# Optimization experiments

Measured on AMD Instinct MI355X. Metric: run time of the kernel, lower is better.

## Reference

```python
import jax, jax.numpy as jnp
import numpy as np

N_VARS = 32
D_MODEL = 256
D_MECH = 128
D_NOISE = D_MODEL // 4
N_LAYERS = 3
TEMP = 0.5
BATCH = 512


def gelu(x):
    return jax.nn.gelu(x, approximate=False)  # torch nn.GELU default is exact erf


def setup_inputs() -> dict:
    key = jax.random.key(0)
    ks = jax.random.split(key, 12)
    n, d, m, dn = N_VARS, D_MODEL, D_MECH, D_NOISE
    return {
        "exogenous_noise": jax.random.normal(ks[0], (BATCH, n, dn), dtype=jnp.float32),
        # learned params (edge_logits init randn*0.5 for a nontrivial adjacency)
        "edge_logits": jax.random.normal(ks[1], (n, n), dtype=jnp.float32) * 0.5,
        "var_emb": jax.random.normal(ks[2], (n, d), dtype=jnp.float32) * 0.02,
        # shared parent_aggregate Linear(d, d); weights stored [in, out]
        "pa_W": jax.random.normal(ks[3], (d, d), dtype=jnp.float32) / np.sqrt(d).astype(np.float32),
        "pa_b": jnp.zeros((d,), dtype=jnp.float32),
        # per-variable mechanism MLP weights, stacked on variable axis
        "m_W1": jax.random.normal(ks[4], (n, d, m), dtype=jnp.float32) / np.sqrt(d).astype(np.float32),
        "m_b1": jnp.zeros((n, m), dtype=jnp.float32),
        "m_W2": jax.random.normal(ks[5], (n, m, m), dtype=jnp.float32) / np.sqrt(m).astype(np.float32),
        "m_b2": jnp.zeros((n, m), dtype=jnp.float32),
        "m_W3": jax.random.normal(ks[6], (n, m, d), dtype=jnp.float32) / np.sqrt(m).astype(np.float32),
        "m_b3": jnp.zeros((n, d), dtype=jnp.float32),
        # per-variable noise encoder Linear(dn, d)
        "ne_W": jax.random.normal(ks[7], (n, dn, d), dtype=jnp.float32) / np.sqrt(dn).astype(np.float32),
        "ne_b": jnp.zeros((n, d), dtype=jnp.float32),
    }


def _forward(exogenous_noise, edge_logits, var_emb, pa_W, pa_b,
             m_W1, m_b1, m_W2, m_b2, m_W3, m_b3, ne_W, ne_b):
    n, d = N_VARS, D_MODEL
    batch = exogenous_noise.shape[0]
    # eval-mode adjacency: sigmoid(masked_logits / temp); diagonal masked out
    diag_mask = 1.0 - jnp.eye(n, dtype=edge_logits.dtype)
    adj = jax.nn.sigmoid((edge_logits * diag_mask) / jnp.asarray(TEMP, edge_logits.dtype))
    adj_cols = adj.T                                  # row i = adj[:, i], parents of var i
    noise_t = jnp.transpose(exogenous_noise, (1, 0, 2))  # (n, batch, dn)

    values0 = jnp.zeros((batch, n, d), dtype=exogenous_noise.dtype)
    idx = jnp.arange(n)
    xs = (idx, adj_cols, var_emb, noise_t, m_W1, m_b1, m_W2, m_b2, m_W3, m_b3, ne_W, ne_b)

    def var_step(values, x):
        i, a_col, emb_i, nz, w1, b1, w2, b2, w3, b3, nw, nb = x
        # adjacency-weighted aggregation over ALL current values (sequentially updated)
        pc = jnp.einsum('v,bvd->bd', a_col, values)
        parent_input = gelu((pc + emb_i) @ pa_W + pa_b)
        h = gelu(parent_input @ w1 + b1)
        h = gelu(h @ w2 + b2)
        out = h @ w3 + b3
        out = out + gelu(nz @ nw + nb)               # noise encoder contribution
        values = values.at[:, i].set(out)
        return values, None

    values = values0
    for _ in range(N_LAYERS):
        values, _ = jax.lax.scan(var_step, values, xs)
    return values


def reference(exogenous_noise, edge_logits, var_emb, pa_W, pa_b,
              m_W1, m_b1, m_W2, m_b2, m_W3, m_b3, ne_W, ne_b):
    return _forward(exogenous_noise, edge_logits, var_emb, pa_W, pa_b,
                    m_W1, m_b1, m_W2, m_b2, m_W3, m_b3, ne_W, ne_b)
```

## Files before the change

kernel.cpp:

```cpp
#include <hip/hip_runtime.h>


typedef __bf16 bf16x8 __attribute__((ext_vector_type(8)));
typedef float  f32x4  __attribute__((ext_vector_type(4)));

#define N_VARS 32
#define BTILE 4
#define NBLK 128

#define WS_ADJB   0
#define WS_B3P    4096
#define WS_EMBP   36864
#define WS_WSB    69632
#define ELOFF_PA  0
#define ELOFF_W1  65536
#define ELOFF_W2  1114112
#define ELOFF_W3  1638400
#define ELOFF_W3P 2686976
#define WS_NE2    7540736

#define XSTR 272
#define HSTR 144
#define VSTR 40

__device__ __forceinline__ unsigned short f2b(float f) {
    unsigned u = __float_as_uint(f);
    u += 0x7FFFu + ((u >> 16) & 1u);
    return (unsigned short)(u >> 16);
}

__device__ __forceinline__ float b2f(unsigned short u) {
    return __uint_as_float(((unsigned)u) << 16);
}

__device__ __forceinline__ void bar_lds() {
    asm volatile("s_waitcnt lgkmcnt(0)\n\ts_barrier" ::: "memory");
}

__device__ __forceinline__ float gelu_e(float x) {
    float z  = x * 0.7071067811865476f;
    float az = fabsf(z);
    float t  = __builtin_amdgcn_rcpf(1.0f + 0.47047f * az);
    float p  = t * (0.3480242f + t * (-0.0958798f + t * 0.7478556f));
    float e  = 1.0f - p * __expf(-z * z);
    float er = (z < 0.0f) ? -e : e;
    return 0.5f * x * (1.0f + er);
}

__device__ __forceinline__ float pickq(f32x4 v, int q) {
    float lo = (q & 1) ? v[1] : v[0];
    float hi = (q & 1) ? v[3] : v[2];
    return (q & 2) ? hi : lo;
}
__device__ __forceinline__ float pick4(float x0, float x1, float x2, float x3, int q) {
    float lo = (q & 1) ? x1 : x0;
    float hi = (q & 1) ? x3 : x2;
    return (q & 2) ? hi : lo;
}

#define MFMA16(a, b, c) __builtin_amdgcn_mfma_f32_16x16x32_bf16(a, b, c, 0, 0, 0)

__global__ void prep_lin(const float* __restrict__ paW, const float* __restrict__ mW3,
                         const float* __restrict__ mb3, const float* __restrict__ emb,
                         const float* __restrict__ pab,
                         float* __restrict__ tmpf, float* __restrict__ b3P,
                         float* __restrict__ embP) {
    const int b = blockIdx.x, d = threadIdx.x;
    if (b < 512) {
        const int v = b >> 4, mg = (b & 15) * 8;
        const float* w3r = mW3 + (size_t)(v * 128 + mg) * 256;
        float acc[8];
        #pragma unroll
        for (int r = 0; r < 8; r++) acc[r] = 0.f;
        for (int n = 0; n < 256; n++) {
            float pa = paW[n * 256 + d];
            #pragma unroll
            for (int r = 0; r < 8; r++) acc[r] += w3r[r * 256 + n] * pa;
        }
        #pragma unroll
        for (int r = 0; r < 8; r++)
            tmpf[(size_t)(v * 128 + mg + r) * 256 + d] = acc[r];
    } else if (b < 544) {
        const int v = b - 512;
        float a = 0.f;
        for (int n = 0; n < 256; n++) a += mb3[v * 256 + n] * paW[n * 256 + d];
        b3P[v * 256 + d] = a;
    } else {
        const int v = b - 544;
        float a = pab[d];
        for (int n = 0; n < 256; n++) a += emb[v * 256 + n] * paW[n * 256 + d];
        embP[v * 256 + d] = a;
    }
}

__global__ void prep_all(const float* __restrict__ paW, const float* __restrict__ mW1,
                         const float* __restrict__ mW2, const float* __restrict__ mW3,
                         const float* __restrict__ edge, unsigned short* __restrict__ wsb,
                         unsigned short* __restrict__ adjb,
                         const float* __restrict__ noise, const float* __restrict__ neW,
                         const float* __restrict__ neb, float* __restrict__ outp,
                         const float* __restrict__ tmpf) {
    __shared__ unsigned short tile[32 * 256];
    const int c = blockIdx.x, tid = threadIdx.x;
    if (c < 648) {
        const float* src; unsigned short* dst; int N, KS, ks;
        if (c < 8)        { src = paW;                     dst = wsb + ELOFF_PA;              N = 256; KS = 8; ks = c; }
        else if (c < 264) { int v = (c - 8) >> 3;   ks = (c - 8) & 7;
                            src = mW1 + v * 32768;         dst = wsb + ELOFF_W1 + v * 32768;  N = 128; KS = 8; }
        else if (c < 392) { int v = (c - 264) >> 2; ks = (c - 264) & 3;
                            src = mW2 + v * 16384;         dst = wsb + ELOFF_W2 + v * 16384;  N = 128; KS = 4; }
        else if (c < 520) { int v = (c - 392) >> 2; ks = (c - 392) & 3;
                            src = mW3 + v * 32768;         dst = wsb + ELOFF_W3 + v * 32768;  N = 256; KS = 4; }
        else              { int v = (c - 520) >> 2; ks = (c - 520) & 3;
                            src = tmpf + v * 32768;        dst = wsb + ELOFF_W3P + v * 32768; N = 256; KS = 4; }
        const int kb = ks * 32, nsh = (N == 256) ? 8 : 7;
        for (int t = tid; t < 32 * N; t += 256) {
            int r = t >> nsh, col = t & (N - 1);
            tile[r * N + col] = f2b(src[(kb + r) * N + col]);
        }
        __syncthreads();
        const int nout = (N >> 4) * 64;
        for (int o = tid; o < nout; o += 256) {
            int nt = o >> 6, lane = o & 63;
            int n = nt * 16 + (lane & 15), k0 = (lane >> 4) << 3;
            unsigned e[8];
            #pragma unroll
            for (int j = 0; j < 8; j++) e[j] = tile[(k0 + j) * N + n];
            uint4 pk;
            pk.x = e[0] | (e[1] << 16); pk.y = e[2] | (e[3] << 16);
            pk.z = e[4] | (e[5] << 16); pk.w = e[6] | (e[7] << 16);
            *(uint4*)(dst + ((nt * KS + ks) * 64 + lane) * 8) = pk;
        }
    } else if (c == 648) {
        for (int t = tid; t < 1024; t += 256) {
            int v = t >> 5, ci = t & 31;
            float x = edge[t];
            float m = (v == ci) ? 0.0f : x;
            float a = __builtin_amdgcn_rcpf(1.0f + __expf(-2.0f * m));
            unsigned short hi = f2b(a);
            float rem = a - b2f(hi);
            adjb[ci * 64 + v]      = hi;
            adjb[ci * 64 + 32 + v] = f2b(rem);
        }
    } else {
        int sb = c - 649;
        int i = sb >> 5, g = sb & 31, d = tid;
        float w[64];
        #pragma unroll
        for (int k = 0; k < 64; k++) w[k] = neW[(i * 64 + k) * 256 + d];
        float bias = neb[i * 256 + d];
        for (int bb = 0; bb < 16; bb++) {
            int b = g * 16 + bb;
            const float* nr = noise + (b * 32 + i) * 64;
            float a0 = bias, a1 = 0.f, a2 = 0.f, a3 = 0.f;
            #pragma unroll
            for (int k = 0; k < 16; k++) {
                a0 += nr[4 * k + 0] * w[4 * k + 0];
                a1 += nr[4 * k + 1] * w[4 * k + 1];
                a2 += nr[4 * k + 2] * w[4 * k + 2];
                a3 += nr[4 * k + 3] * w[4 * k + 3];
            }
            outp[(b * 32 + i) * 256 + d] = gelu_e((a0 + a1) + (a2 + a3));
        }
    }
}

__global__ void prep_ne2(const float* __restrict__ nep, const __bf16* __restrict__ wsbf,
                         unsigned short* __restrict__ ne2) {
    const int tid = threadIdx.x;
    const int wid = tid >> 6, lane = tid & 63, l15 = lane & 15, q = lane >> 4;
    const int gt = blockIdx.x * 4 + wid;
    const int rowbase = gt * 16;
    bf16x8 afr[8];
    #pragma unroll
    for (int ks = 0; ks < 8; ks++) {
        const float* s = nep + (size_t)(rowbase + l15) * 256 + ks * 32 + q * 8;
        float4 x0 = *(const float4*)s;
        float4 x1 = *(const float4*)(s + 4);
        uint4 pk;
        pk.x = (unsigned)f2b(x0.x) | ((unsigned)f2b(x0.y) << 16);
        pk.y = (unsigned)f2b(x0.z) | ((unsigned)f2b(x0.w) << 16);
        pk.z = (unsigned)f2b(x1.x) | ((unsigned)f2b(x1.y) << 16);
        pk.w = (unsigned)f2b(x1.z) | ((unsigned)f2b(x1.w) << 16);
        afr[ks] = __builtin_bit_cast(bf16x8, pk);
    }
    #pragma unroll 4
    for (int nt = 0; nt < 16; nt++) {
        f32x4 e4 = {0, 0, 0, 0}, o4 = {0, 0, 0, 0};
        #pragma unroll
        for (int ks = 0; ks < 8; ks += 2) {
            bf16x8 b0 = *(const bf16x8*)(wsbf + ELOFF_PA + ((nt * 8 + ks) * 64 + lane) * 8);
            bf16x8 b1 = *(const bf16x8*)(wsbf + ELOFF_PA + ((nt * 8 + ks + 1) * 64 + lane) * 8);
            e4 = MFMA16(afr[ks], b0, e4);
            o4 = MFMA16(afr[ks + 1], b1, o4);
        }
        f32x4 a = e4 + o4;
        #pragma unroll
        for (int r = 0; r < 4; r++)
            ne2[(size_t)(rowbase + 4 * q + r) * 256 + nt * 16 + l15] = f2b(a[r]);
    }
}

__global__ __launch_bounds__(512) void
scm_main(const float* __restrict__ embP, const float* __restrict__ b3Pp,
         const float* __restrict__ mb1, const float* __restrict__ mb2,
         const float* __restrict__ mb3, const unsigned short* __restrict__ adjb,
         const __bf16* __restrict__ wsbf, const unsigned short* __restrict__ ne2,
         float* __restrict__ outp) {
    __shared__ unsigned short valsP[1024 * VSTR];
    __shared__ unsigned short X2[4 * XSTR];
    __shared__ unsigned short Hs1[4 * HSTR];
    __shared__ unsigned short Hs2[4 * HSTR];

    const int tid = threadIdx.x, blk = blockIdx.x;

    {
        uint4 z; z.x = z.y = z.z = z.w = 0;
        for (int k = tid; k < 5120; k += 512) ((uint4*)valsP)[k] = z;
    }

    const int wid = tid >> 6, lane = tid & 63, l15 = lane & 15, q = lane >> 4;
    const int l3 = l15 & 3;
    const int nW = wid * 16 + l15;
    const int n0 = nW, n1 = nW + 128;

    X2[q * XSTR + n0] = f2b(gelu_e(embP[n0]));
    X2[q * XSTR + n1] = f2b(gelu_e(embP[n1]));
    bar_lds();

    for (int s = 0; s < 3 * N_VARS; s++) {
        const int i = s & 31, ni = (s + 1) & 31;
        const bool last = s >= 64;

        float bi1 = mb1[i * 128 + nW];
        float bi2 = mb2[i * 128 + nW];
        bf16x8 w1f[8];
        #pragma unroll
        for (int ks = 0; ks < 8; ks++)
            w1f[ks] = *(const bf16x8*)(wsbf + ELOFF_W1 + (size_t)i * 32768 +
                                       ((wid * 8 + ks) * 64 + lane) * 8);
        bf16x8 w2f[4], wPf0[4], wPf1[4];
        #pragma unroll
        for (int ks = 0; ks < 4; ks++) {
            w2f[ks]  = *(const bf16x8*)(wsbf + ELOFF_W2 + (size_t)i * 16384 +
                                        ((wid * 4 + ks) * 64 + lane) * 8);
            wPf0[ks] = *(const bf16x8*)(wsbf + ELOFF_W3P + (size_t)i * 32768 +
                                        ((wid * 4 + ks) * 64 + lane) * 8);
            wPf1[ks] = *(const bf16x8*)(wsbf + ELOFF_W3P + (size_t)i * 32768 +
                                        (((wid + 8) * 4 + ks) * 64 + lane) * 8);
        }
        const size_t nrow = ((size_t)(blk * BTILE + q) * 32 + i) * 256;
        const float ne2_0 = b2f(ne2[nrow + n0]);
        const float ne2_1 = b2f(ne2[nrow + n1]);
        const float b3P0 = b3Pp[i * 256 + n0];
        const float b3P1 = b3Pp[i * 256 + n1];
        const float eP0 = embP[ni * 256 + n0];
        const float eP1 = embP[ni * 256 + n1];
        bf16x8 anh = *(const bf16x8*)(adjb + ni * 64 + q * 8);
        bf16x8 anl = *(const bf16x8*)(adjb + ni * 64 + 32 + q * 8);
        const float ani = b2f(adjb[ni * 64 + i]) + b2f(adjb[ni * 64 + 32 + i]);
        bf16x8 w3f0[4], w3f1[4];
        float b3a = 0.f, b3b = 0.f, neq0 = 0.f, neq1 = 0.f;
        if (last) {
            #pragma unroll
            for (int ks = 0; ks < 4; ks++) {
                w3f0[ks] = *(const bf16x8*)(wsbf + ELOFF_W3 + (size_t)i * 32768 +
                                            ((wid * 4 + ks) * 64 + lane) * 8);
                w3f1[ks] = *(const bf16x8*)(wsbf + ELOFF_W3 + (size_t)i * 32768 +
                                            (((wid + 8) * 4 + ks) * 64 + lane) * 8);
            }
            b3a = mb3[i * 256 + n0];
            b3b = mb3[i * 256 + n1];
            neq0 = outp[nrow + n0];
            neq1 = outp[nrow + n1];
        }

        {
            f32x4 aa = {0, 0, 0, 0}, ab = {0, 0, 0, 0};
            f32x4 ac = {0, 0, 0, 0}, ad = {0, 0, 0, 0};
            #pragma unroll
            for (int ks = 0; ks < 8; ks += 4) {
                bf16x8 af0 = *(const bf16x8*)(X2 + l3 * XSTR + ks * 32 + q * 8);
                bf16x8 af1 = *(const bf16x8*)(X2 + l3 * XSTR + (ks + 1) * 32 + q * 8);
                bf16x8 af2 = *(const bf16x8*)(X2 + l3 * XSTR + (ks + 2) * 32 + q * 8);
                bf16x8 af3 = *(const bf16x8*)(X2 + l3 * XSTR + (ks + 3) * 32 + q * 8);
                aa = MFMA16(af0, w1f[ks], aa);
                ab = MFMA16(af1, w1f[ks + 1], ab);
                ac = MFMA16(af2, w1f[ks + 2], ac);
                ad = MFMA16(af3, w1f[ks + 3], ad);
            }
            float sb = (pickq(aa, q) + pickq(ab, q)) +
                       (pickq(ac, q) + pickq(ad, q)) + bi1;
            Hs1[q * HSTR + nW] = f2b(gelu_e(sb));
        }
        bar_lds();

        f32x4 P0[4], P1[4];
        float oP0, oP1;
        {
            f32x4 ca = {0, 0, 0, 0}, cb = {0, 0, 0, 0};
            #pragma unroll
            for (int ks = 0; ks < 4; ks += 2) {
                bf16x8 af0 = *(const bf16x8*)(Hs1 + l3 * HSTR + ks * 32 + q * 8);
                bf16x8 af1 = *(const bf16x8*)(Hs1 + l3 * HSTR + (ks + 1) * 32 + q * 8);
                ca = MFMA16(af0, w2f[ks], ca);
                cb = MFMA16(af1, w2f[ks + 1], cb);
            }
            #pragma unroll
            for (int t = 0; t < 4; t++) {
                bf16x8 vf0 = *(const bf16x8*)(valsP + (t * 256 + n0) * VSTR + q * 8);
                bf16x8 vf1 = *(const bf16x8*)(valsP + (t * 256 + n1) * VSTR + q * 8);
                f32x4 z = {0, 0, 0, 0};
                P0[t] = MFMA16(anl, vf0, MFMA16(anh, vf0, z));
                P1[t] = MFMA16(anl, vf1, MFMA16(anh, vf1, z));
            }
            oP0 = b2f(valsP[(q * 256 + n0) * VSTR + i]);
            oP1 = b2f(valsP[(q * 256 + n1) * VSTR + i]);
            float scv = pickq(ca, q) + pickq(cb, q) + bi2;
            Hs2[q * HSTR + nW] = f2b(gelu_e(scv));
        }
        bar_lds();

        {
            f32x4 c0a = {0, 0, 0, 0}, c0b = {0, 0, 0, 0};
            f32x4 c1a = {0, 0, 0, 0}, c1b = {0, 0, 0, 0};
            #pragma unroll
            for (int ks = 0; ks < 4; ks += 2) {
                bf16x8 af0 = *(const bf16x8*)(Hs2 + l3 * HSTR + ks * 32 + q * 8);
                bf16x8 af1 = *(const bf16x8*)(Hs2 + l3 * HSTR + (ks + 1) * 32 + q * 8);
                c0a = MFMA16(af0, wPf0[ks], c0a);
                c1a = MFMA16(af0, wPf1[ks], c1a);
                c0b = MFMA16(af1, wPf0[ks + 1], c0b);
                c1b = MFMA16(af1, wPf1[ks + 1], c1b);
            }
            float nP0 = pickq(c0a, q) + pickq(c0b, q) + b3P0 + ne2_0;
            float nP1 = pickq(c1a, q) + pickq(c1b, q) + b3P1 + ne2_1;
            unsigned short ur0 = f2b(nP0), ur1 = f2b(nP1);
            valsP[(q * 256 + n0) * VSTR + i] = ur0;
            valsP[(q * 256 + n1) * VSTR + i] = ur1;
            float pc0 = pick4(P0[0][0], P0[1][0], P0[2][0], P0[3][0], q);
            float pc1 = pick4(P1[0][0], P1[1][0], P1[2][0], P1[3][0], q);
            float x0 = pc0 + ani * (b2f(ur0) - oP0) + eP0;
            float x1 = pc1 + ani * (b2f(ur1) - oP1) + eP1;
            X2[q * XSTR + n0] = f2b(gelu_e(x0));
            X2[q * XSTR + n1] = f2b(gelu_e(x1));
            if (last) {
                f32x4 d0a = {0, 0, 0, 0}, d0b = {0, 0, 0, 0};
                f32x4 d1a = {0, 0, 0, 0}, d1b = {0, 0, 0, 0};
                #pragma unroll
                for (int ks = 0; ks < 4; ks += 2) {
                    bf16x8 af0 = *(const bf16x8*)(Hs2 + l3 * HSTR + ks * 32 + q * 8);
                    bf16x8 af1 = *(const bf16x8*)(Hs2 + l3 * HSTR + (ks + 1) * 32 + q * 8);
                    d0a = MFMA16(af0, w3f0[ks], d0a);
                    d1a = MFMA16(af0, w3f1[ks], d1a);
                    d0b = MFMA16(af1, w3f0[ks + 1], d0b);
                    d1b = MFMA16(af1, w3f1[ks + 1], d1b);
                }
                outp[nrow + n0] = pickq(d0a, q) + pickq(d0b, q) + b3a + neq0;
                outp[nrow + n1] = pickq(d1a, q) + pickq(d1b, q) + b3b + neq1;
            }
        }
        bar_lds();
    }
}

extern "C" void kernel_launch(void* const* d_in, const int* in_sizes, int n_in,
                              void* d_out, int out_size, void* d_ws, size_t ws_size,
                              hipStream_t stream) {
    (void)in_sizes; (void)n_in; (void)out_size; (void)ws_size;
    const float* noise = (const float*)d_in[0];
    const float* edge  = (const float*)d_in[1];
    const float* emb   = (const float*)d_in[2];
    const float* paW   = (const float*)d_in[3];
    const float* pab   = (const float*)d_in[4];
    const float* mW1   = (const float*)d_in[5];
    const float* mb1   = (const float*)d_in[6];
    const float* mW2   = (const float*)d_in[7];
    const float* mb2   = (const float*)d_in[8];
    const float* mW3   = (const float*)d_in[9];
    const float* mb3   = (const float*)d_in[10];
    const float* neW   = (const float*)d_in[11];
    const float* neb   = (const float*)d_in[12];
    float* outp = (float*)d_out;

    unsigned short* adjb = (unsigned short*)((char*)d_ws + WS_ADJB);
    float* b3P  = (float*)((char*)d_ws + WS_B3P);
    float* embP = (float*)((char*)d_ws + WS_EMBP);
    unsigned short* wsb  = (unsigned short*)((char*)d_ws + WS_WSB);
    float* tmpf = (float*)((char*)d_ws + WS_NE2);
    unsigned short* ne2u = (unsigned short*)((char*)d_ws + WS_NE2);

    prep_lin<<<576, 256, 0, stream>>>(paW, mW3, mb3, emb, pab, tmpf, b3P, embP);
    prep_all<<<1673, 256, 0, stream>>>(paW, mW1, mW2, mW3, edge, wsb, adjb,
                                       noise, neW, neb, outp, tmpf);
    prep_ne2<<<256, 256, 0, stream>>>(outp, (const __bf16*)wsb, ne2u);
    scm_main<<<NBLK, 512, 0, stream>>>(embP, b3P, mb1, mb2, mb3, adjb,
                                       (const __bf16*)wsb, ne2u, outp);
}
```

Measured before the change: 424.1 us.

## Merge prep_lin into prep_all and double-buffer per-variable weights in main loop

Folds the W3·paW product, the b3 and embedding projections into the single prep_all launch, writing the W3P product straight into the MFMA fragment layout in bf16 and dropping the fp32 tmp buffer and one kernel launch. In the sequential 96-step main loop, the next variable's W1/W2/W3P fragments are prefetched into a second register set while the current step runs, so global weight-load latency is hidden behind compute. This doubles weight register usage, which may raise register pressure or cause spills.

```diff
diff --git a/kernel.cpp b/kernel.cpp
--- a/kernel.cpp
+++ b/kernel.cpp
@@ -60,59 +60,26 @@
 
 #define MFMA16(a, b, c) __builtin_amdgcn_mfma_f32_16x16x32_bf16(a, b, c, 0, 0, 0)
 
-__global__ void prep_lin(const float* __restrict__ paW, const float* __restrict__ mW3,
-                         const float* __restrict__ mb3, const float* __restrict__ emb,
-                         const float* __restrict__ pab,
-                         float* __restrict__ tmpf, float* __restrict__ b3P,
-                         float* __restrict__ embP) {
-    const int b = blockIdx.x, d = threadIdx.x;
-    if (b < 512) {
-        const int v = b >> 4, mg = (b & 15) * 8;
-        const float* w3r = mW3 + (size_t)(v * 128 + mg) * 256;
-        float acc[8];
-        #pragma unroll
-        for (int r = 0; r < 8; r++) acc[r] = 0.f;
-        for (int n = 0; n < 256; n++) {
-            float pa = paW[n * 256 + d];
-            #pragma unroll
-            for (int r = 0; r < 8; r++) acc[r] += w3r[r * 256 + n] * pa;
-        }
-        #pragma unroll
-        for (int r = 0; r < 8; r++)
-            tmpf[(size_t)(v * 128 + mg + r) * 256 + d] = acc[r];
-    } else if (b < 544) {
-        const int v = b - 512;
-        float a = 0.f;
-        for (int n = 0; n < 256; n++) a += mb3[v * 256 + n] * paW[n * 256 + d];
-        b3P[v * 256 + d] = a;
-    } else {
-        const int v = b - 544;
-        float a = pab[d];
-        for (int n = 0; n < 256; n++) a += emb[v * 256 + n] * paW[n * 256 + d];
-        embP[v * 256 + d] = a;
-    }
-}
-
 __global__ void prep_all(const float* __restrict__ paW, const float* __restrict__ mW1,
                          const float* __restrict__ mW2, const float* __restrict__ mW3,
                          const float* __restrict__ edge, unsigned short* __restrict__ wsb,
                          unsigned short* __restrict__ adjb,
                          const float* __restrict__ noise, const float* __restrict__ neW,
                          const float* __restrict__ neb, float* __restrict__ outp,
-                         const float* __restrict__ tmpf) {
+                         const float* __restrict__ mb3, const float* __restrict__ emb,
+                         const float* __restrict__ pab,
+                         float* __restrict__ b3P, float* __restrict__ embP) {
     __shared__ unsigned short tile[32 * 256];
     const int c = blockIdx.x, tid = threadIdx.x;
-    if (c < 648) {
+    if (c < 520) {
         const float* src; unsigned short* dst; int N, KS, ks;
-        if (c < 8)        { src = paW;                     dst = wsb + ELOFF_PA;              N = 256; KS = 8; ks = c; }
+        if (c < 8)        { src = paW;                     dst = wsb + ELOFF_PA;             N = 256; KS = 8; ks = c; }
         else if (c < 264) { int v = (c - 8) >> 3;   ks = (c - 8) & 7;
-                            src = mW1 + v * 32768;         dst = wsb + ELOFF_W1 + v * 32768;  N = 128; KS = 8; }
+                            src = mW1 + v * 32768;         dst = wsb + ELOFF_W1 + v * 32768; N = 128; KS = 8; }
         else if (c < 392) { int v = (c - 264) >> 2; ks = (c - 264) & 3;
-                            src = mW2 + v * 16384;         dst = wsb + ELOFF_W2 + v * 16384;  N = 128; KS = 4; }
-        else if (c < 520) { int v = (c - 392) >> 2; ks = (c - 392) & 3;
-                            src = mW3 + v * 32768;         dst = wsb + ELOFF_W3 + v * 32768;  N = 256; KS = 4; }
-        else              { int v = (c - 520) >> 2; ks = (c - 520) & 3;
-                            src = tmpf + v * 32768;        dst = wsb + ELOFF_W3P + v * 32768; N = 256; KS = 4; }
+                            src = mW2 + v * 16384;         dst = wsb + ELOFF_W2 + v * 16384; N = 128; KS = 4; }
+        else              { int v = (c - 392) >> 2; ks = (c - 392) & 3;
+                            src = mW3 + v * 32768;         dst = wsb + ELOFF_W3 + v * 32768; N = 256; KS = 4; }
         const int kb = ks * 32, nsh = (N == 256) ? 8 : 7;
         for (int t = tid; t < 32 * N; t += 256) {
             int r = t >> nsh, col = t & (N - 1);
@@ -131,7 +98,7 @@
             pk.z = e[4] | (e[5] << 16); pk.w = e[6] | (e[7] << 16);
             *(uint4*)(dst + ((nt * KS + ks) * 64 + lane) * 8) = pk;
         }
-    } else if (c == 648) {
+    } else if (c == 520) {
         for (int t = tid; t < 1024; t += 256) {
             int v = t >> 5, ci = t & 31;
             float x = edge[t];
@@ -142,8 +109,8 @@
             adjb[ci * 64 + v]      = hi;
             adjb[ci * 64 + 32 + v] = f2b(rem);
         }
-    } else {
-        int sb = c - 649;
+    } else if (c < 1545) {
+        int sb = c - 521;
         int i = sb >> 5, g = sb & 31, d = tid;
         float w[64];
         #pragma unroll
@@ -162,6 +129,37 @@
             }
             outp[(b * 32 + i) * 256 + d] = gelu_e((a0 + a1) + (a2 + a3));
         }
+    } else if (c < 2057) {
+        const int idx = c - 1545;
+        const int v = idx >> 4, mg = (idx & 15) * 8;
+        const int d = tid;
+        const float* w3r = mW3 + (size_t)(v * 128 + mg) * 256;
+        float acc[8];
+        #pragma unroll
+        for (int r = 0; r < 8; r++) acc[r] = 0.f;
+        for (int n = 0; n < 256; n++) {
+            float pa = paW[n * 256 + d];
+            #pragma unroll
+            for (int r = 0; r < 8; r++) acc[r] += w3r[r * 256 + n] * pa;
+        }
+        const int ks = mg >> 5, lg = (mg >> 3) & 3;
+        const int nt = d >> 4, lane = lg * 16 + (d & 15);
+        uint4 pk;
+        pk.x = (unsigned)f2b(acc[0]) | ((unsigned)f2b(acc[1]) << 16);
+        pk.y = (unsigned)f2b(acc[2]) | ((unsigned)f2b(acc[3]) << 16);
+        pk.z = (unsigned)f2b(acc[4]) | ((unsigned)f2b(acc[5]) << 16);
+        pk.w = (unsigned)f2b(acc[6]) | ((unsigned)f2b(acc[7]) << 16);
+        *(uint4*)(wsb + ELOFF_W3P + v * 32768 + ((nt * 4 + ks) * 64 + lane) * 8) = pk;
+    } else if (c < 2089) {
+        const int v = c - 2057;
+        float a = 0.f;
+        for (int n = 0; n < 256; n++) a += mb3[v * 256 + n] * paW[n * 256 + tid];
+        b3P[v * 256 + tid] = a;
+    } else {
+        const int v = c - 2089;
+        float a = pab[tid];
+        for (int n = 0; n < 256; n++) a += emb[v * 256 + n] * paW[n * 256 + tid];
+        embP[v * 256 + tid] = a;
     }
 }
 
@@ -228,27 +226,37 @@
     X2[q * XSTR + n1] = f2b(gelu_e(embP[n1]));
     bar_lds();
 
-    for (int s = 0; s < 3 * N_VARS; s++) {
+    bf16x8 wa1[8], wa2[4], waP0[4], waP1[4];
+    bf16x8 wb1[8], wb2[4], wbP0[4], wbP1[4];
+
+    auto loadw = [&](int i, bf16x8 (&w1)[8], bf16x8 (&w2)[4],
+                     bf16x8 (&wP0)[4], bf16x8 (&wP1)[4]) {
+        #pragma unroll
+        for (int ks = 0; ks < 8; ks++)
+            w1[ks] = *(const bf16x8*)(wsbf + ELOFF_W1 + (size_t)i * 32768 +
+                                      ((wid * 8 + ks) * 64 + lane) * 8);
+        #pragma unroll
+        for (int ks = 0; ks < 4; ks++) {
+            w2[ks]  = *(const bf16x8*)(wsbf + ELOFF_W2 + (size_t)i * 16384 +
+                                       ((wid * 4 + ks) * 64 + lane) * 8);
+            wP0[ks] = *(const bf16x8*)(wsbf + ELOFF_W3P + (size_t)i * 32768 +
+                                       ((wid * 4 + ks) * 64 + lane) * 8);
+            wP1[ks] = *(const bf16x8*)(wsbf + ELOFF_W3P + (size_t)i * 32768 +
+                                       (((wid + 8) * 4 + ks) * 64 + lane) * 8);
+        }
+    };
+
+    auto step = [&](int s, bf16x8 (&w1f)[8], bf16x8 (&w2f)[4],
+                    bf16x8 (&wPf0)[4], bf16x8 (&wPf1)[4],
+                    bf16x8 (&x1)[8], bf16x8 (&x2)[4],
+                    bf16x8 (&xP0)[4], bf16x8 (&xP1)[4]) {
         const int i = s & 31, ni = (s + 1) & 31;
         const bool last = s >= 64;
 
+        loadw(ni, x1, x2, xP0, xP1);
+
         float bi1 = mb1[i * 128 + nW];
         float bi2 = mb2[i * 128 + nW];
-        bf16x8 w1f[8];
-        #pragma unroll
-        for (int ks = 0; ks < 8; ks++)
-            w1f[ks] = *(const bf16x8*)(wsbf + ELOFF_W1 + (size_t)i * 32768 +
-                                       ((wid * 8 + ks) * 64 + lane) * 8);
-        bf16x8 w2f[4], wPf0[4], wPf1[4];
-        #pragma unroll
-        for (int ks = 0; ks < 4; ks++) {
-            w2f[ks]  = *(const bf16x8*)(wsbf + ELOFF_W2 + (size_t)i * 16384 +
-                                        ((wid * 4 + ks) * 64 + lane) * 8);
-            wPf0[ks] = *(const bf16x8*)(wsbf + ELOFF_W3P + (size_t)i * 32768 +
-                                        ((wid * 4 + ks) * 64 + lane) * 8);
-            wPf1[ks] = *(const bf16x8*)(wsbf + ELOFF_W3P + (size_t)i * 32768 +
-                                        (((wid + 8) * 4 + ks) * 64 + lane) * 8);
-        }
         const size_t nrow = ((size_t)(blk * BTILE + q) * 32 + i) * 256;
         const float ne2_0 = b2f(ne2[nrow + n0]);
         const float ne2_1 = b2f(ne2[nrow + n1]);
@@ -361,6 +369,12 @@
             }
         }
         bar_lds();
+    };
+
+    loadw(0, wa1, wa2, waP0, waP1);
+    for (int ss = 0; ss < 48; ss++) {
+        step(2 * ss,     wa1, wa2, waP0, waP1, wb1, wb2, wbP0, wbP1);
+        step(2 * ss + 1, wb1, wb2, wbP0, wbP1, wa1, wa2, waP0, waP1);
     }
 }
 
@@ -387,12 +401,11 @@
     float* b3P  = (float*)((char*)d_ws + WS_B3P);
     float* embP = (float*)((char*)d_ws + WS_EMBP);
     unsigned short* wsb  = (unsigned short*)((char*)d_ws + WS_WSB);
-    float* tmpf = (float*)((char*)d_ws + WS_NE2);
     unsigned short* ne2u = (unsigned short*)((char*)d_ws + WS_NE2);
 
-    prep_lin<<<576, 256, 0, stream>>>(paW, mW3, mb3, emb, pab, tmpf, b3P, embP);
-    prep_all<<<1673, 256, 0, stream>>>(paW, mW1, mW2, mW3, edge, wsb, adjb,
-                                       noise, neW, neb, outp, tmpf);
+    prep_all<<<2121, 256, 0, stream>>>(paW, mW1, mW2, mW3, edge, wsb, adjb,
+                                       noise, neW, neb, outp, mb3, emb, pab,
+                                       b3P, embP);
     prep_ne2<<<256, 256, 0, stream>>>(outp, (const __bf16*)wsb, ne2u);
     scm_main<<<NBLK, 512, 0, stream>>>(embP, b3P, mb1, mb2, mb3, adjb,
                                        (const __bf16*)wsb, ne2u, outp);
```

New measurement: 514.2 us. 1.21x slower.
